# Performance work log

Measured on AMD Instinct MI355X. Metric: run time of the kernel, lower is better.

## Reference

```python
import jax, jax.numpy as jnp
import numpy as np

B, T_PAST, FUTURE_N = 128, 1024, 512
IN_F, IP, H, OUT_F = 64, 128, 256, 64


def _init(key, shape, fan_in):
    return (jax.random.uniform(key, shape, jnp.float32) * 2.0 - 1.0) / np.sqrt(fan_in).astype(np.float32)


def setup_inputs() -> dict:
    key = jax.random.key(0)
    ks = jax.random.split(key, 16)
    return {
        "x": jax.random.normal(ks[0], (B, T_PAST, IN_F), jnp.float32),
        "future_n": FUTURE_N,
        # encoder: Linear(IN_F -> IP)
        "enc_W": _init(ks[1], (IP, IN_F), IN_F),
        "enc_b": _init(ks[2], (IP,), IN_F),
        # future encoder: Linear(H -> IP)
        "fut_W": _init(ks[3], (IP, H), H),
        "fut_b": _init(ks[4], (IP,), H),
        # decoder: Linear(H -> OUT_F)
        "dec_W": _init(ks[5], (OUT_F, H), H),
        "dec_b": _init(ks[6], (OUT_F,), H),
        # past LSTMCell(IP, H)
        "pW_ih": _init(ks[7], (4 * H, IP), H),
        "pW_hh": _init(ks[8], (4 * H, H), H),
        "pb_ih": _init(ks[9], (4 * H,), H),
        "pb_hh": _init(ks[10], (4 * H,), H),
        # future LSTMCell(IP, H)
        "fW_ih": _init(ks[11], (4 * H, IP), H),
        "fW_hh": _init(ks[12], (4 * H, H), H),
        "fb_ih": _init(ks[13], (4 * H,), H),
        "fb_hh": _init(ks[14], (4 * H,), H),
    }


def _lstm_cell(xt, h, c, W_ih, W_hh, b_ih, b_hh):
    # torch LSTMCell gate order: i, f, g, o
    gates = xt @ W_ih.T + h @ W_hh.T + (b_ih + b_hh)
    i, f, g, o = jnp.split(gates, 4, axis=-1)
    c_new = jax.nn.sigmoid(f) * c + jax.nn.sigmoid(i) * jnp.tanh(g)
    h_new = jax.nn.sigmoid(o) * jnp.tanh(c_new)
    return h_new, c_new


def reference(x, future_n, enc_W, enc_b, fut_W, fut_b, dec_W, dec_b,
              pW_ih, pW_hh, pb_ih, pb_hh, fW_ih, fW_hh, fb_ih, fb_hh):
    batch = x.shape[0]
    hidden = pW_hh.shape[1]
    h0 = jnp.zeros((batch, hidden), x.dtype)
    c0 = jnp.zeros((batch, hidden), x.dtype)

    encoded = x @ enc_W.T + enc_b  # [B, T, IP]

    def past_step(carry, xt):
        h, c = carry
        h, c = _lstm_cell(xt, h, c, pW_ih, pW_hh, pb_ih, pb_hh)
        return (h, c), h

    (h, c), hs_past = jax.lax.scan(past_step, (h0, c0), jnp.swapaxes(encoded, 0, 1))

    def fut_step(carry, _):
        h, c = carry
        inp = h @ fut_W.T + fut_b
        h, c = _lstm_cell(inp, h, c, fW_ih, fW_hh, fb_ih, fb_hh)
        return (h, c), h

    _, hs_fut = jax.lax.scan(fut_step, (h, c), None, length=future_n)

    hs = jnp.concatenate([hs_past, hs_fut], axis=0)  # [T+F, B, H]
    out = jnp.swapaxes(hs, 0, 1) @ dec_W.T + dec_b  # [B, T+F, OUT_F]
    return out
```

## Files before the change

kernel.cpp:

```cpp
#include <hip/hip_runtime.h>

#define B_    128
#define TPAST 1024
#define FN    512
#define TT    1536
#define INF   64
#define IPF   128
#define HD    256
#define NG    1024
#define OUTF  64

typedef _Float16 f16;
typedef _Float16 f16x8 __attribute__((ext_vector_type(8)));
typedef _Float16 f16x4 __attribute__((ext_vector_type(4)));
typedef float    f32x4 __attribute__((ext_vector_type(4)));

template<int N> struct ic { static constexpr int value = N; };

__device__ __forceinline__ float sigm_(float x) {
  return __builtin_amdgcn_rcpf(1.f + __expf(-x));
}
__device__ __forceinline__ float tanh_(float x) {
  return 1.f - 2.f * __builtin_amdgcn_rcpf(1.f + __expf(2.f * x));
}
__device__ __forceinline__ f16x8 oload16(const f16* p) {
  f16x8 v;
  asm volatile("global_load_dwordx4 %0, %1, off\n\ts_waitcnt vmcnt(0)"
               : "=v"(v) : "v"(p));
  return v;
}

extern "C" __global__ void eprep(
    const float* __restrict__ enc_W, const float* __restrict__ enc_b,
    const float* __restrict__ fut_W, const float* __restrict__ fut_b,
    const float* __restrict__ dec_W,
    const float* __restrict__ pW_ih, const float* __restrict__ pW_hh,
    const float* __restrict__ pb_ih, const float* __restrict__ pb_hh,
    const float* __restrict__ fW_ih, const float* __restrict__ fW_hh,
    const float* __restrict__ fb_ih, const float* __restrict__ fb_hh,
    f16* __restrict__ Wp_in, float* __restrict__ bp,
    f16* __restrict__ Wp16, f16* __restrict__ Wf16,
    float* __restrict__ bf, f16* __restrict__ dW16)
{
  int stride = gridDim.x * blockDim.x;
  int gid = blockIdx.x * blockDim.x + threadIdx.x;
  for (int i = gid; i < NG * HD; i += stride) {
    int n = i >> 8, j = i & 255;
    float s = fW_hh[i];
    for (int m = 0; m < IPF; ++m) s += fW_ih[n * IPF + m] * fut_W[m * HD + j];
    Wf16[i] = (f16)s;
    Wp16[i] = (f16)pW_hh[i];
  }
  for (int i = gid; i < NG * INF; i += stride) {
    int n = i >> 6, k = i & 63;
    float s = 0.f;
    for (int m = 0; m < IPF; ++m) s += pW_ih[n * IPF + m] * enc_W[m * INF + k];
    Wp_in[i] = (f16)s;
  }
  for (int i = gid; i < OUTF * HD; i += stride) dW16[i] = (f16)dec_W[i];
  for (int n = gid; n < NG; n += stride) {
    float s1 = pb_ih[n] + pb_hh[n], s2 = fb_ih[n] + fb_hh[n];
    for (int m = 0; m < IPF; ++m) {
      s1 += pW_ih[n * IPF + m] * enc_b[m];
      s2 += fW_ih[n * IPF + m] * fut_b[m];
    }
    bp[n] = s1; bf[n] = s2;
  }
}

extern "C" __global__ __launch_bounds__(64) void epgemm(
    const float* __restrict__ x, const f16* __restrict__ Wp_in,
    const float* __restrict__ bp, f16* __restrict__ P, int t0, int Tc)
{
  int wg = blockIdx.x;
  int tl = wg >> 3, bt = wg & 7;
  int t = t0 + tl;
  int l = (int)threadIdx.x, r = l & 15, g = l >> 4;
  const float* xb = x + ((size_t)(bt * 16 + r) * TPAST + t) * INF;
  f16x8 a[2];
#pragma unroll
  for (int kk = 0; kk < 2; ++kk) {
    const float* px = xb + kk * 32 + g * 8;
    f32x4 v0 = *(const f32x4*)px;
    f32x4 v1 = *(const f32x4*)(px + 4);
#pragma unroll
    for (int e = 0; e < 4; ++e) { a[kk][e] = (f16)v0[e]; a[kk][4 + e] = (f16)v1[e]; }
  }
  for (int nt = 0; nt < 64; ++nt) {
    int n = nt * 16 + r;
    f16x8 w0 = *(const f16x8*)(Wp_in + (size_t)n * INF + g * 8);
    f16x8 w1 = *(const f16x8*)(Wp_in + (size_t)n * INF + 32 + g * 8);
    f32x4 acc = {0.f, 0.f, 0.f, 0.f};
    acc = __builtin_amdgcn_mfma_f32_16x16x32_f16(w0, a[0], acc, 0, 0, 0);
    acc = __builtin_amdgcn_mfma_f32_16x16x32_f16(w1, a[1], acc, 0, 0, 0);
    f32x4 bias4 = *(const f32x4*)&bp[nt * 16 + 4 * g];
    f16x4 hv;
#pragma unroll
    for (int e = 0; e < 4; ++e) hv[e] = (f16)(acc[e] + bias4[e]);
    int ga = nt >> 4, jhp = (nt >> 3) & 1;
    int nl = ga * 128 + (nt & 7) * 16 + 4 * g;
    f16* Pt = P + (((size_t)(jhp * 8 + bt) * Tc + tl) * 16 + r) * 512;
    *(f16x4*)(Pt + nl) = hv;
  }
}

extern "C" __global__ __launch_bounds__(256, 1)
void erecur(
    const f16* __restrict__ W, const f16* __restrict__ P, int pstep,
    const float* __restrict__ bias,
    f16* __restrict__ hs, f16* __restrict__ h_state, float* __restrict__ c_state,
    f16* __restrict__ Hx, unsigned int* __restrict__ flags,
    int Tc, int seq0, int init_state)
{
  __shared__ f16  Wl[512 * 96];
  __shared__ f16  hb[2][16 * 128];
  __shared__ float cb[128 * 20];
  __shared__ f16  bl[512];

  int tid = (int)threadIdx.x;
  int w = tid >> 6, l = tid & 63, r = l & 15, g = l >> 4;
  int wg = blockIdx.x;
  int bs = wg & 7, jh = wg >> 3;
  int b0 = bs * 16;
  int pwg = wg ^ 8;

  for (int nl = tid; nl < 512; nl += 256) {
    int ng = (nl >> 7) * 256 + jh * 128 + (nl & 127);
#pragma unroll
    for (int c8 = 0; c8 < 12; ++c8) {
      f16x8 v = *(const f16x8*)(W + (size_t)ng * HD + 160 + c8 * 8);
      *(f16x8*)&Wl[(nl * 96 + c8 * 8) ^ ((nl & 7) << 3)] = v;
    }
  }
  if (bias) {
    for (int i = tid; i < 512; i += 256) {
      int ng = (i >> 7) * 256 + jh * 128 + (i & 127);
      bl[i] = (f16)bias[ng];
    }
  }
  f16x8 wf[4][2][5];
#pragma unroll
  for (int ga = 0; ga < 4; ++ga)
#pragma unroll
    for (int s = 0; s < 2; ++s) {
      int ng = ga * 256 + jh * 128 + w * 32 + s * 16 + r;
#pragma unroll
      for (int kt = 0; kt < 5; ++kt)
        wf[ga][s][kt] = oload16(W + (size_t)ng * HD + kt * 32 + g * 8);
    }
  int cur0 = seq0 & 1;
  f16x8 pa[4];
  if (init_state) {
    for (int i = tid; i < 16 * 128; i += 256) {
      int b = i >> 7, jl = i & 127;
      hb[cur0][(b * 128 + jl) ^ ((b & 7) << 3)] = (f16)0.f;
    }
    for (int i = tid; i < 128 * 20; i += 256) cb[i] = 0.f;
    f16x8 z = {};
#pragma unroll
    for (int kt = 0; kt < 4; ++kt) pa[kt] = z;
  } else {
    for (int i = tid; i < 16 * 128; i += 256) {
      int b = i >> 7, jl = i & 127;
      hb[cur0][(b * 128 + jl) ^ ((b & 7) << 3)] =
          h_state[(size_t)(b0 + b) * HD + jh * 128 + jl];
    }
    for (int i = tid; i < 16 * 128; i += 256) {
      int b = i >> 7, jl = i & 127;
      cb[jl * 20 + b] = c_state[(size_t)(b0 + b) * HD + jh * 128 + jl];
    }
#pragma unroll
    for (int kt = 0; kt < 4; ++kt)
      pa[kt] = *(const f16x8*)(h_state + (size_t)(b0 + r) * HD + (jh ^ 1) * 128 + kt * 32 + g * 8);
  }
  const f16* Pw = P ? (P + (size_t)wg * Tc * pstep) : nullptr;
  f16x4 pvA[4][2], pvB[4][2];
  if (P) {
#pragma unroll
    for (int ga = 0; ga < 4; ++ga)
#pragma unroll
      for (int s = 0; s < 2; ++s)
        pvA[ga][s] = *(const f16x4*)(Pw + r * 512 + ga * 128 + w * 32 + s * 16 + 4 * g);
  }
  __syncthreads();

  for (int tl = 0; tl < Tc; ++tl) {
    int v = seq0 + tl;
    const f16* hbc = hb[v & 1];

    f32x4 acc[4][2];
#pragma unroll
    for (int ga = 0; ga < 4; ++ga)
#pragma unroll
      for (int s = 0; s < 2; ++s) acc[ga][s] = f32x4{0.f, 0.f, 0.f, 0.f};

    auto do_kt = [&](auto ktc, f16x8 hfrag) {
      constexpr int KT = decltype(ktc)::value;
#pragma unroll
      for (int ga = 0; ga < 4; ++ga)
#pragma unroll
        for (int s = 0; s < 2; ++s) {
          if constexpr (KT < 5) {
            acc[ga][s] = __builtin_amdgcn_mfma_f32_16x16x32_f16(wf[ga][s][KT], hfrag, acc[ga][s], 0, 0, 0);
          } else {
            int nl = ga * 128 + w * 32 + s * 16 + r;
            f16x8 aw = *(const f16x8*)&Wl[(nl * 96 + (KT - 5) * 32 + g * 8) ^ ((nl & 7) << 3)];
            acc[ga][s] = __builtin_amdgcn_mfma_f32_16x16x32_f16(aw, hfrag, acc[ga][s], 0, 0, 0);
          }
        }
    };
    auto ownfrag = [&](int ktl) {
      return *(const f16x8*)&hbc[(r * 128 + ktl * 32 + g * 8) ^ ((r & 7) << 3)];
    };

    if (jh == 0) {
      do_kt(ic<0>{}, ownfrag(0)); do_kt(ic<1>{}, ownfrag(1));
      do_kt(ic<2>{}, ownfrag(2)); do_kt(ic<3>{}, ownfrag(3));
    } else {
      do_kt(ic<4>{}, ownfrag(0)); do_kt(ic<5>{}, ownfrag(1));
      do_kt(ic<6>{}, ownfrag(2)); do_kt(ic<7>{}, ownfrag(3));
    }

    if (tl > 0) {
      while (__hip_atomic_load(&flags[pwg], __ATOMIC_ACQUIRE,
                               __HIP_MEMORY_SCOPE_AGENT) < (unsigned)v)
        __builtin_amdgcn_s_sleep(1);
      const f16* HxR = Hx + ((size_t)(v & 1) * 16 + pwg) * 2048;
#pragma unroll
      for (int kt = 0; kt < 4; ++kt)
        pa[kt] = *(const f16x8*)(HxR + r * 128 + kt * 32 + g * 8);
    }
    if (P && tl + 1 < Tc) {
#pragma unroll
      for (int ga = 0; ga < 4; ++ga)
#pragma unroll
        for (int s = 0; s < 2; ++s)
          pvB[ga][s] = *(const f16x4*)(Pw + pstep + r * 512 + ga * 128 + w * 32 + s * 16 + 4 * g);
    }
    if (jh == 0) {
      do_kt(ic<4>{}, pa[0]); do_kt(ic<5>{}, pa[1]);
      do_kt(ic<6>{}, pa[2]); do_kt(ic<7>{}, pa[3]);
    } else {
      do_kt(ic<0>{}, pa[0]); do_kt(ic<1>{}, pa[1]);
      do_kt(ic<2>{}, pa[2]); do_kt(ic<3>{}, pa[3]);
    }

    f16* hbn = hb[(v + 1) & 1];
    f16* HxW = Hx + ((size_t)((v + 1) & 1) * 16 + wg) * 2048;
#pragma unroll
    for (int s = 0; s < 2; ++s) {
      int j4 = w * 32 + s * 16 + 4 * g;
      float cold[4];
#pragma unroll
      for (int e = 0; e < 4; ++e) cold[e] = cb[(j4 + e) * 20 + r];
      f16x4 b4[4];
      if (!P) {
#pragma unroll
        for (int ga = 0; ga < 4; ++ga) b4[ga] = *(const f16x4*)&bl[ga * 128 + j4];
      }
      union { unsigned long long u; f16 h4[4]; } pk;
#pragma unroll
      for (int e = 0; e < 4; ++e) {
        float xi = acc[0][s][e], xf = acc[1][s][e], xg = acc[2][s][e], xo = acc[3][s][e];
        if (P) {
          xi += (float)pvA[0][s][e]; xf += (float)pvA[1][s][e];
          xg += (float)pvA[2][s][e]; xo += (float)pvA[3][s][e];
        } else {
          xi += (float)b4[0][e]; xf += (float)b4[1][e];
          xg += (float)b4[2][e]; xo += (float)b4[3][e];
        }
        float ii = sigm_(xi), ff = sigm_(xf), oo = sigm_(xo), gg = tanh_(xg);
        float cn = ff * cold[e] + ii * gg;
        cb[(j4 + e) * 20 + r] = cn;
        pk.h4[e] = (f16)(oo * tanh_(cn));
      }
      __hip_atomic_store((unsigned long long*)(HxW + r * 128 + j4), pk.u,
                         __ATOMIC_RELAXED, __HIP_MEMORY_SCOPE_AGENT);
      *(unsigned long long*)&hbn[(r * 128 + j4) ^ ((r & 7) << 3)] = pk.u;
    }
    __syncthreads();

    if (tid == 0)
      __hip_atomic_store(&flags[wg], (unsigned)(v + 1),
                         __ATOMIC_RELEASE, __HIP_MEMORY_SCOPE_AGENT);

    {
      int b = tid >> 4, seg = tid & 15;
      f16x8 hv = *(const f16x8*)&hbn[(b * 128 + seg * 8) ^ ((b & 7) << 3)];
      *(f16x8*)(hs + ((size_t)tl * B_ + b0 + b) * HD + jh * 128 + seg * 8) = hv;
    }
    if (P) {
#pragma unroll
      for (int ga = 0; ga < 4; ++ga)
#pragma unroll
        for (int s = 0; s < 2; ++s) pvA[ga][s] = pvB[ga][s];
      Pw += pstep;
    }
  }
  {
    const f16* hbf = hb[(seq0 + Tc) & 1];
    int b = tid >> 4, seg = tid & 15;
    f16x8 hv = *(const f16x8*)&hbf[(b * 128 + seg * 8) ^ ((b & 7) << 3)];
    *(f16x8*)(h_state + (size_t)(b0 + b) * HD + jh * 128 + seg * 8) = hv;
  }
  for (int i = tid; i < 16 * 128; i += 256) {
    int b = i >> 7, jl = i & 127;
    c_state[(size_t)(b0 + b) * HD + jh * 128 + jl] = cb[jl * 20 + b];
  }
}

extern "C" __global__ __launch_bounds__(64) void edec(
    const f16* __restrict__ hs, const f16* __restrict__ dW,
    const float* __restrict__ dec_b, float* __restrict__ out, int t0, int Tc)
{
  int wg = blockIdx.x;
  int tt = wg >> 7, b = wg & 127;
  int l = (int)threadIdx.x, r = l & 15, g = l >> 4;
  f16x8 wfr[4][8];
#pragma unroll
  for (int nt = 0; nt < 4; ++nt)
#pragma unroll
    for (int kt = 0; kt < 8; ++kt)
      wfr[nt][kt] = *(const f16x8*)(dW + (size_t)(nt * 16 + r) * HD + kt * 32 + g * 8);
  float bb[4];
#pragma unroll
  for (int nt = 0; nt < 4; ++nt) bb[nt] = dec_b[nt * 16 + r];
  f32x4 acc[2][4];
  const f32x4 zero4 = {0.f, 0.f, 0.f, 0.f};
#pragma unroll
  for (int mt = 0; mt < 2; ++mt)
#pragma unroll
    for (int nt = 0; nt < 4; ++nt) acc[mt][nt] = zero4;
#pragma unroll
  for (int mt = 0; mt < 2; ++mt)
#pragma unroll
    for (int kt = 0; kt < 8; ++kt) {
      f16x8 a = *(const f16x8*)(hs + ((size_t)(tt * 32 + mt * 16 + r) * B_ + b) * HD + kt * 32 + g * 8);
#pragma unroll
      for (int nt = 0; nt < 4; ++nt)
        acc[mt][nt] = __builtin_amdgcn_mfma_f32_16x16x32_f16(a, wfr[nt][kt], acc[mt][nt], 0, 0, 0);
    }
#pragma unroll
  for (int mt = 0; mt < 2; ++mt)
#pragma unroll
    for (int nt = 0; nt < 4; ++nt)
#pragma unroll
      for (int e = 0; e < 4; ++e) {
        int t = t0 + tt * 32 + mt * 16 + 4 * g + e;
        out[((size_t)b * TT + t) * OUTF + nt * 16 + r] = acc[mt][nt][e] + bb[nt];
      }
}

extern "C" void kernel_launch(void* const* d_in, const int* in_sizes, int n_in,
                              void* d_out, int out_size, void* d_ws, size_t ws_size,
                              hipStream_t stream)
{
  const float* x     = (const float*)d_in[0];
  const float* enc_W = (const float*)d_in[2];
  const float* enc_b = (const float*)d_in[3];
  const float* fut_W = (const float*)d_in[4];
  const float* fut_b = (const float*)d_in[5];
  const float* dec_W = (const float*)d_in[6];
  const float* dec_b = (const float*)d_in[7];
  const float* pW_ih = (const float*)d_in[8];
  const float* pW_hh = (const float*)d_in[9];
  const float* pb_ih = (const float*)d_in[10];
  const float* pb_hh = (const float*)d_in[11];
  const float* fW_ih = (const float*)d_in[12];
  const float* fW_hh = (const float*)d_in[13];
  const float* fb_ih = (const float*)d_in[14];
  const float* fb_hh = (const float*)d_in[15];
  (void)in_sizes; (void)n_in; (void)out_size;

  char* p = (char*)d_ws;
  auto alloc = [&](size_t bytes) { char* q = p; p += (bytes + 255) & ~(size_t)255; return q; };
  f16*   Wp_in = (f16*)  alloc((size_t)NG * INF * 2);
  float* bp    = (float*)alloc((size_t)NG * 4);
  f16*   Wp16  = (f16*)  alloc((size_t)NG * HD * 2);
  f16*   Wf16  = (f16*)  alloc((size_t)NG * HD * 2);
  float* bfb   = (float*)alloc((size_t)NG * 4);
  f16*   dW16  = (f16*)  alloc((size_t)OUTF * HD * 2);
  f16*   h_st  = (f16*)  alloc((size_t)B_ * HD * 2);
  float* c_st  = (float*)alloc((size_t)B_ * HD * 4);
  f16*   Hx    = (f16*)  alloc((size_t)2 * 16 * 2048 * 2);
  unsigned int* flags = (unsigned int*)alloc(64);
  size_t fixed = (size_t)(p - (char*)d_ws);

  auto need = [&](int rr) {
    size_t pp = (size_t)(rr < TPAST ? rr : TPAST) * NG * B_ * 2;
    size_t hh = (size_t)rr * B_ * HD * 2;
    return pp + hh + 4096;
  };
  size_t avail = ws_size > fixed ? ws_size - fixed : 0;
  int R = 128;
  if (avail >= need(1536)) R = 1536;
  else if (avail >= need(512)) R = 512;
  else if (avail >= need(256)) R = 256;

  f16* Pbuf = (f16*)alloc((size_t)(R < TPAST ? R : TPAST) * NG * B_ * 2);
  f16* HS   = (f16*)alloc((size_t)R * B_ * HD * 2);

  hipMemsetAsync(flags, 0, 64, stream);

  eprep<<<512, 256, 0, stream>>>(enc_W, enc_b, fut_W, fut_b, dec_W,
                                 pW_ih, pW_hh, pb_ih, pb_hh,
                                 fW_ih, fW_hh, fb_ih, fb_hh,
                                 Wp_in, bp, Wp16, Wf16, bfb, dW16);

  for (int t0 = 0; t0 < TPAST; t0 += R) {
    int Tc = (TPAST - t0) < R ? (TPAST - t0) : R;
    epgemm<<<Tc * 8, 64, 0, stream>>>(x, Wp_in, bp, Pbuf, t0, Tc);
    erecur<<<16, 256, 0, stream>>>(Wp16, Pbuf, 512 * 16, nullptr, HS, h_st, c_st,
                                   Hx, flags, Tc, t0, t0 == 0 ? 1 : 0);
    edec<<<(Tc / 32) * B_, 64, 0, stream>>>(HS, dW16, dec_b, (float*)d_out, t0, Tc);
  }
  for (int t0 = TPAST; t0 < TT; t0 += R) {
    int Tc = (TT - t0) < R ? (TT - t0) : R;
    erecur<<<16, 256, 0, stream>>>(Wf16, nullptr, 0, bfb, HS, h_st, c_st,
                                   Hx, flags, Tc, t0, 0);
    edec<<<(Tc / 32) * B_, 64, 0, stream>>>(HS, dW16, dec_b, (float*)d_out, t0, Tc);
  }
}
```

Measured before the change: 6.783 ms.

## Halve recurrence workgroups, each handling two batch groups with interleaved sync

The recurrent kernel now runs 8 active workgroups instead of 16. Each one processes two 16-row batch groups per step, alternating between them so one group's compute overlaps the partner-flag wait of the other. The cell state moves from LDS into registers. The projection buffer layout changes so each lane loads its gate preactivations contiguously. The cost is double the serial work per workgroup and loss of the next-step P prefetch, in exchange for fewer participants in the cross-WG handshake and latency hiding between groups.

```diff
diff --git a/kernel.cpp b/kernel.cpp
--- a/kernel.cpp
+++ b/kernel.cpp
@@ -97,10 +97,9 @@
     f16x4 hv;
 #pragma unroll
     for (int e = 0; e < 4; ++e) hv[e] = (f16)(acc[e] + bias4[e]);
-    int ga = nt >> 4, jhp = (nt >> 3) & 1;
-    int nl = ga * 128 + (nt & 7) * 16 + 4 * g;
-    f16* Pt = P + (((size_t)(jhp * 8 + bt) * Tc + tl) * 16 + r) * 512;
-    *(f16x4*)(Pt + nl) = hv;
+    int ga = nt >> 4, jhp = (nt >> 3) & 1, wc = (nt >> 1) & 3, sc = nt & 1;
+    f16* Pt = P + ((size_t)(jhp * 8 + bt) * Tc + tl) * 8192;
+    *(f16x4*)(Pt + ((ga * 8 + sc * 4 + wc) * 64 + l) * 4) = hv;
   }
 }
 
@@ -112,16 +111,15 @@
     f16* __restrict__ Hx, unsigned int* __restrict__ flags,
     int Tc, int seq0, int init_state)
 {
-  __shared__ f16  Wl[512 * 96];
-  __shared__ f16  hb[2][16 * 128];
-  __shared__ float cb[128 * 20];
-  __shared__ f16  bl[512];
+  __shared__ f16 Wl[512 * 96];
+  __shared__ f16 hbG[2][2][16 * 128];
+  __shared__ f16 bl[512];
 
   int tid = (int)threadIdx.x;
   int w = tid >> 6, l = tid & 63, r = l & 15, g = l >> 4;
   int wg = blockIdx.x;
-  int bs = wg & 7, jh = wg >> 3;
-  int b0 = bs * 16;
+  int bp4 = wg & 7, jh = wg >> 3;
+  if (bp4 >= 4) return;
   int pwg = wg ^ 8;
 
   for (int nl = tid; nl < 512; nl += 256) {
@@ -149,164 +147,170 @@
         wf[ga][s][kt] = oload16(W + (size_t)ng * HD + kt * 32 + g * 8);
     }
   int cur0 = seq0 & 1;
-  f16x8 pa[4];
-  if (init_state) {
-    for (int i = tid; i < 16 * 128; i += 256) {
-      int b = i >> 7, jl = i & 127;
-      hb[cur0][(b * 128 + jl) ^ ((b & 7) << 3)] = (f16)0.f;
-    }
-    for (int i = tid; i < 128 * 20; i += 256) cb[i] = 0.f;
-    f16x8 z = {};
-#pragma unroll
-    for (int kt = 0; kt < 4; ++kt) pa[kt] = z;
-  } else {
-    for (int i = tid; i < 16 * 128; i += 256) {
-      int b = i >> 7, jl = i & 127;
-      hb[cur0][(b * 128 + jl) ^ ((b & 7) << 3)] =
-          h_state[(size_t)(b0 + b) * HD + jh * 128 + jl];
-    }
-    for (int i = tid; i < 16 * 128; i += 256) {
-      int b = i >> 7, jl = i & 127;
-      cb[jl * 20 + b] = c_state[(size_t)(b0 + b) * HD + jh * 128 + jl];
-    }
-#pragma unroll
-    for (int kt = 0; kt < 4; ++kt)
-      pa[kt] = *(const f16x8*)(h_state + (size_t)(b0 + r) * HD + (jh ^ 1) * 128 + kt * 32 + g * 8);
-  }
-  const f16* Pw = P ? (P + (size_t)wg * Tc * pstep) : nullptr;
-  f16x4 pvA[4][2], pvB[4][2];
-  if (P) {
-#pragma unroll
-    for (int ga = 0; ga < 4; ++ga)
-#pragma unroll
-      for (int s = 0; s < 2; ++s)
-        pvA[ga][s] = *(const f16x4*)(Pw + r * 512 + ga * 128 + w * 32 + s * 16 + 4 * g);
-  }
+  f32x4 creg[2][2];
+  for (int G = 0; G < 2; ++G) {
+    int b0G = (bp4 * 2 + G) * 16;
+    if (init_state) {
+      for (int i = tid; i < 16 * 128; i += 256) {
+        int b = i >> 7;
+        hbG[G][cur0][i ^ ((b & 7) << 3)] = (f16)0.f;
+      }
+    } else {
+      for (int i = tid; i < 16 * 128; i += 256) {
+        int b = i >> 7, jl = i & 127;
+        hbG[G][cur0][i ^ ((b & 7) << 3)] =
+            h_state[(size_t)(b0G + b) * HD + jh * 128 + jl];
+      }
+    }
+  }
+#pragma unroll
+  for (int G = 0; G < 2; ++G)
+#pragma unroll
+    for (int s = 0; s < 2; ++s) {
+      int b0G = (bp4 * 2 + G) * 16;
+      int j4 = w * 32 + s * 16 + 4 * g;
+      if (init_state) creg[G][s] = f32x4{0.f, 0.f, 0.f, 0.f};
+      else creg[G][s] = *(const f32x4*)&c_state[(size_t)(b0G + r) * HD + jh * 128 + j4];
+    }
   __syncthreads();
 
   for (int tl = 0; tl < Tc; ++tl) {
     int v = seq0 + tl;
-    const f16* hbc = hb[v & 1];
-
-    f32x4 acc[4][2];
-#pragma unroll
-    for (int ga = 0; ga < 4; ++ga)
-#pragma unroll
-      for (int s = 0; s < 2; ++s) acc[ga][s] = f32x4{0.f, 0.f, 0.f, 0.f};
-
-    auto do_kt = [&](auto ktc, f16x8 hfrag) {
-      constexpr int KT = decltype(ktc)::value;
+#pragma unroll
+    for (int G = 0; G < 2; ++G) {
+      int bsG = bp4 * 2 + G;
+      int b0G = bsG * 16;
+      f16x4 pv[4][2];
+      if (P) {
+        const f16* PwG = P + ((size_t)(jh * 8 + bsG) * Tc + tl) * 8192;
+#pragma unroll
+        for (int ga = 0; ga < 4; ++ga)
+#pragma unroll
+          for (int s = 0; s < 2; ++s)
+            pv[ga][s] = *(const f16x4*)(PwG + ((ga * 8 + s * 4 + w) * 64 + l) * 4);
+      }
+      f32x4 acc[4][2];
 #pragma unroll
       for (int ga = 0; ga < 4; ++ga)
 #pragma unroll
-        for (int s = 0; s < 2; ++s) {
-          if constexpr (KT < 5) {
-            acc[ga][s] = __builtin_amdgcn_mfma_f32_16x16x32_f16(wf[ga][s][KT], hfrag, acc[ga][s], 0, 0, 0);
+        for (int s = 0; s < 2; ++s) acc[ga][s] = f32x4{0.f, 0.f, 0.f, 0.f};
+
+      const f16* hbc = hbG[G][v & 1];
+      auto do_kt = [&](auto ktc, f16x8 hfrag) {
+        constexpr int KT = decltype(ktc)::value;
+#pragma unroll
+        for (int ga = 0; ga < 4; ++ga)
+#pragma unroll
+          for (int s = 0; s < 2; ++s) {
+            if constexpr (KT < 5) {
+              acc[ga][s] = __builtin_amdgcn_mfma_f32_16x16x32_f16(wf[ga][s][KT], hfrag, acc[ga][s], 0, 0, 0);
+            } else {
+              int nl = ga * 128 + w * 32 + s * 16 + r;
+              f16x8 aw = *(const f16x8*)&Wl[(nl * 96 + (KT - 5) * 32 + g * 8) ^ ((nl & 7) << 3)];
+              acc[ga][s] = __builtin_amdgcn_mfma_f32_16x16x32_f16(aw, hfrag, acc[ga][s], 0, 0, 0);
+            }
+          }
+      };
+      auto ownfrag = [&](int ktl) {
+        return *(const f16x8*)&hbc[(r * 128 + ktl * 32 + g * 8) ^ ((r & 7) << 3)];
+      };
+
+      if (jh == 0) {
+        do_kt(ic<0>{}, ownfrag(0)); do_kt(ic<1>{}, ownfrag(1));
+        do_kt(ic<2>{}, ownfrag(2)); do_kt(ic<3>{}, ownfrag(3));
+      } else {
+        do_kt(ic<4>{}, ownfrag(0)); do_kt(ic<5>{}, ownfrag(1));
+        do_kt(ic<6>{}, ownfrag(2)); do_kt(ic<7>{}, ownfrag(3));
+      }
+
+      f16x8 pa[4];
+      if (tl == 0) {
+        if (init_state) {
+          f16x8 z = {};
+#pragma unroll
+          for (int kt = 0; kt < 4; ++kt) pa[kt] = z;
+        } else {
+#pragma unroll
+          for (int kt = 0; kt < 4; ++kt)
+            pa[kt] = *(const f16x8*)(h_state + (size_t)(b0G + r) * HD + (jh ^ 1) * 128 + kt * 32 + g * 8);
+        }
+      } else {
+        while (__hip_atomic_load(&flags[pwg * 2 + G], __ATOMIC_ACQUIRE,
+                                 __HIP_MEMORY_SCOPE_AGENT) < (unsigned)v)
+          __builtin_amdgcn_s_sleep(1);
+        const f16* HxR = Hx + ((size_t)(v & 1) * 32 + pwg * 2 + G) * 2048;
+#pragma unroll
+        for (int kt = 0; kt < 4; ++kt)
+          pa[kt] = *(const f16x8*)(HxR + r * 128 + kt * 32 + g * 8);
+      }
+      if (jh == 0) {
+        do_kt(ic<4>{}, pa[0]); do_kt(ic<5>{}, pa[1]);
+        do_kt(ic<6>{}, pa[2]); do_kt(ic<7>{}, pa[3]);
+      } else {
+        do_kt(ic<0>{}, pa[0]); do_kt(ic<1>{}, pa[1]);
+        do_kt(ic<2>{}, pa[2]); do_kt(ic<3>{}, pa[3]);
+      }
+
+      f16* hbn = hbG[G][(v + 1) & 1];
+      f16* HxW = Hx + ((size_t)((v + 1) & 1) * 32 + wg * 2 + G) * 2048;
+#pragma unroll
+      for (int s = 0; s < 2; ++s) {
+        int j4 = w * 32 + s * 16 + 4 * g;
+        f16x4 b4[4];
+        if (!P) {
+#pragma unroll
+          for (int ga = 0; ga < 4; ++ga) b4[ga] = *(const f16x4*)&bl[ga * 128 + j4];
+        }
+        f32x4 cold = creg[G][s], cnew;
+        union { unsigned long long u; f16 h4[4]; } pk;
+#pragma unroll
+        for (int e = 0; e < 4; ++e) {
+          float xi = acc[0][s][e], xf = acc[1][s][e], xg = acc[2][s][e], xo = acc[3][s][e];
+          if (P) {
+            xi += (float)pv[0][s][e]; xf += (float)pv[1][s][e];
+            xg += (float)pv[2][s][e]; xo += (float)pv[3][s][e];
           } else {
-            int nl = ga * 128 + w * 32 + s * 16 + r;
-            f16x8 aw = *(const f16x8*)&Wl[(nl * 96 + (KT - 5) * 32 + g * 8) ^ ((nl & 7) << 3)];
-            acc[ga][s] = __builtin_amdgcn_mfma_f32_16x16x32_f16(aw, hfrag, acc[ga][s], 0, 0, 0);
+            xi += (float)b4[0][e]; xf += (float)b4[1][e];
+            xg += (float)b4[2][e]; xo += (float)b4[3][e];
           }
+          float ii = sigm_(xi), ff = sigm_(xf), oo = sigm_(xo), gg = tanh_(xg);
+          float cn = ff * cold[e] + ii * gg;
+          cnew[e] = cn;
+          pk.h4[e] = (f16)(oo * tanh_(cn));
         }
-    };
-    auto ownfrag = [&](int ktl) {
-      return *(const f16x8*)&hbc[(r * 128 + ktl * 32 + g * 8) ^ ((r & 7) << 3)];
-    };
-
-    if (jh == 0) {
-      do_kt(ic<0>{}, ownfrag(0)); do_kt(ic<1>{}, ownfrag(1));
-      do_kt(ic<2>{}, ownfrag(2)); do_kt(ic<3>{}, ownfrag(3));
-    } else {
-      do_kt(ic<4>{}, ownfrag(0)); do_kt(ic<5>{}, ownfrag(1));
-      do_kt(ic<6>{}, ownfrag(2)); do_kt(ic<7>{}, ownfrag(3));
-    }
-
-    if (tl > 0) {
-      while (__hip_atomic_load(&flags[pwg], __ATOMIC_ACQUIRE,
-                               __HIP_MEMORY_SCOPE_AGENT) < (unsigned)v)
-        __builtin_amdgcn_s_sleep(1);
-      const f16* HxR = Hx + ((size_t)(v & 1) * 16 + pwg) * 2048;
-#pragma unroll
-      for (int kt = 0; kt < 4; ++kt)
-        pa[kt] = *(const f16x8*)(HxR + r * 128 + kt * 32 + g * 8);
-    }
-    if (P && tl + 1 < Tc) {
-#pragma unroll
-      for (int ga = 0; ga < 4; ++ga)
-#pragma unroll
-        for (int s = 0; s < 2; ++s)
-          pvB[ga][s] = *(const f16x4*)(Pw + pstep + r * 512 + ga * 128 + w * 32 + s * 16 + 4 * g);
-    }
-    if (jh == 0) {
-      do_kt(ic<4>{}, pa[0]); do_kt(ic<5>{}, pa[1]);
-      do_kt(ic<6>{}, pa[2]); do_kt(ic<7>{}, pa[3]);
-    } else {
-      do_kt(ic<0>{}, pa[0]); do_kt(ic<1>{}, pa[1]);
-      do_kt(ic<2>{}, pa[2]); do_kt(ic<3>{}, pa[3]);
-    }
-
-    f16* hbn = hb[(v + 1) & 1];
-    f16* HxW = Hx + ((size_t)((v + 1) & 1) * 16 + wg) * 2048;
-#pragma unroll
-    for (int s = 0; s < 2; ++s) {
-      int j4 = w * 32 + s * 16 + 4 * g;
-      float cold[4];
-#pragma unroll
-      for (int e = 0; e < 4; ++e) cold[e] = cb[(j4 + e) * 20 + r];
-      f16x4 b4[4];
-      if (!P) {
-#pragma unroll
-        for (int ga = 0; ga < 4; ++ga) b4[ga] = *(const f16x4*)&bl[ga * 128 + j4];
-      }
-      union { unsigned long long u; f16 h4[4]; } pk;
-#pragma unroll
-      for (int e = 0; e < 4; ++e) {
-        float xi = acc[0][s][e], xf = acc[1][s][e], xg = acc[2][s][e], xo = acc[3][s][e];
-        if (P) {
-          xi += (float)pvA[0][s][e]; xf += (float)pvA[1][s][e];
-          xg += (float)pvA[2][s][e]; xo += (float)pvA[3][s][e];
-        } else {
-          xi += (float)b4[0][e]; xf += (float)b4[1][e];
-          xg += (float)b4[2][e]; xo += (float)b4[3][e];
-        }
-        float ii = sigm_(xi), ff = sigm_(xf), oo = sigm_(xo), gg = tanh_(xg);
-        float cn = ff * cold[e] + ii * gg;
-        cb[(j4 + e) * 20 + r] = cn;
-        pk.h4[e] = (f16)(oo * tanh_(cn));
-      }
-      __hip_atomic_store((unsigned long long*)(HxW + r * 128 + j4), pk.u,
-                         __ATOMIC_RELAXED, __HIP_MEMORY_SCOPE_AGENT);
-      *(unsigned long long*)&hbn[(r * 128 + j4) ^ ((r & 7) << 3)] = pk.u;
-    }
-    __syncthreads();
-
-    if (tid == 0)
-      __hip_atomic_store(&flags[wg], (unsigned)(v + 1),
-                         __ATOMIC_RELEASE, __HIP_MEMORY_SCOPE_AGENT);
-
-    {
-      int b = tid >> 4, seg = tid & 15;
-      f16x8 hv = *(const f16x8*)&hbn[(b * 128 + seg * 8) ^ ((b & 7) << 3)];
-      *(f16x8*)(hs + ((size_t)tl * B_ + b0 + b) * HD + jh * 128 + seg * 8) = hv;
-    }
-    if (P) {
-#pragma unroll
-      for (int ga = 0; ga < 4; ++ga)
-#pragma unroll
-        for (int s = 0; s < 2; ++s) pvA[ga][s] = pvB[ga][s];
-      Pw += pstep;
-    }
-  }
-  {
-    const f16* hbf = hb[(seq0 + Tc) & 1];
+        creg[G][s] = cnew;
+        __hip_atomic_store((unsigned long long*)(HxW + r * 128 + j4), pk.u,
+                           __ATOMIC_RELAXED, __HIP_MEMORY_SCOPE_AGENT);
+        *(unsigned long long*)&hbn[(r * 128 + j4) ^ ((r & 7) << 3)] = pk.u;
+      }
+      __syncthreads();
+
+      if (tid == 0)
+        __hip_atomic_store(&flags[wg * 2 + G], (unsigned)(v + 1),
+                           __ATOMIC_RELEASE, __HIP_MEMORY_SCOPE_AGENT);
+
+      {
+        int b = tid >> 4, seg = tid & 15;
+        f16x8 hv = *(const f16x8*)&hbn[(b * 128 + seg * 8) ^ ((b & 7) << 3)];
+        *(f16x8*)(hs + ((size_t)tl * B_ + b0G + b) * HD + jh * 128 + seg * 8) = hv;
+      }
+    }
+  }
+  for (int G = 0; G < 2; ++G) {
+    int b0G = (bp4 * 2 + G) * 16;
+    const f16* hbf = hbG[G][(seq0 + Tc) & 1];
     int b = tid >> 4, seg = tid & 15;
     f16x8 hv = *(const f16x8*)&hbf[(b * 128 + seg * 8) ^ ((b & 7) << 3)];
-    *(f16x8*)(h_state + (size_t)(b0 + b) * HD + jh * 128 + seg * 8) = hv;
-  }
-  for (int i = tid; i < 16 * 128; i += 256) {
-    int b = i >> 7, jl = i & 127;
-    c_state[(size_t)(b0 + b) * HD + jh * 128 + jl] = cb[jl * 20 + b];
-  }
+    *(f16x8*)(h_state + (size_t)(b0G + b) * HD + jh * 128 + seg * 8) = hv;
+  }
+#pragma unroll
+  for (int G = 0; G < 2; ++G)
+#pragma unroll
+    for (int s = 0; s < 2; ++s) {
+      int b0G = (bp4 * 2 + G) * 16;
+      int j4 = w * 32 + s * 16 + 4 * g;
+      *(f32x4*)&c_state[(size_t)(b0G + r) * HD + jh * 128 + j4] = creg[G][s];
+    }
 }
 
 extern "C" __global__ __launch_bounds__(64) void edec(
@@ -382,8 +386,8 @@
   f16*   dW16  = (f16*)  alloc((size_t)OUTF * HD * 2);
   f16*   h_st  = (f16*)  alloc((size_t)B_ * HD * 2);
   float* c_st  = (float*)alloc((size_t)B_ * HD * 4);
-  f16*   Hx    = (f16*)  alloc((size_t)2 * 16 * 2048 * 2);
-  unsigned int* flags = (unsigned int*)alloc(64);
+  f16*   Hx    = (f16*)  alloc((size_t)2 * 32 * 2048 * 2);
+  unsigned int* flags = (unsigned int*)alloc(128);
   size_t fixed = (size_t)(p - (char*)d_ws);
 
   auto need = [&](int rr) {
@@ -400,7 +404,7 @@
   f16* Pbuf = (f16*)alloc((size_t)(R < TPAST ? R : TPAST) * NG * B_ * 2);
   f16* HS   = (f16*)alloc((size_t)R * B_ * HD * 2);
 
-  hipMemsetAsync(flags, 0, 64, stream);
+  hipMemsetAsync(flags, 0, 128, stream);
 
   eprep<<<512, 256, 0, stream>>>(enc_W, enc_b, fut_W, fut_b, dec_W,
                                  pW_ih, pW_hh, pb_ih, pb_hh,
@@ -410,7 +414,7 @@
   for (int t0 = 0; t0 < TPAST; t0 += R) {
     int Tc = (TPAST - t0) < R ? (TPAST - t0) : R;
     epgemm<<<Tc * 8, 64, 0, stream>>>(x, Wp_in, bp, Pbuf, t0, Tc);
-    erecur<<<16, 256, 0, stream>>>(Wp16, Pbuf, 512 * 16, nullptr, HS, h_st, c_st,
+    erecur<<<16, 256, 0, stream>>>(Wp16, Pbuf, 8192, nullptr, HS, h_st, c_st,
                                    Hx, flags, Tc, t0, t0 == 0 ? 1 : 0);
     edec<<<(Tc / 32) * B_, 64, 0, stream>>>(HS, dW16, dec_b, (float*)d_out, t0, Tc);
   }
```

Measured after the change: 11.38 ms. 67.8% more time.
